# Kernel optimization log

Measured on AMD Instinct MI355X. Metric: run time of the kernel, lower is better.

## Reference

```python
import jax, jax.numpy as jnp
import numpy as np

TREE_DEPTH = 10
TOTAL = 2 ** (TREE_DEPTH + 1) - 1  # 2047 nodes per tree
G = 64                              # graphs per batch
N = G * TOTAL                       # 131008 nodes
E = 2 * N                           # 262016 directed edges
H = 256                             # h_dim
HALF = H // 2
L = 4                               # num_layers
LABELS = 32
OUT = 32
BN_EPS = 1e-5
LN_EPS = 1e-5


def setup_inputs() -> dict:
    key = jax.random.key(0)
    ks = jax.random.split(key, 16)
    x = jnp.stack([jax.random.randint(ks[0], (N,), 0, TOTAL),
                   jax.random.randint(ks[1], (N,), 0, LABELS)], axis=1)
    edge_src = jax.random.randint(ks[2], (E,), 0, N)
    edge_dst = jax.random.randint(ks[3], (E,), 0, N)
    edge_weight = jax.random.uniform(ks[4], (E,), dtype=jnp.float32)
    batch = jnp.arange(N, dtype=jnp.int64) // TOTAL          # node -> graph id
    root_index = jnp.arange(G, dtype=jnp.int64) * TOTAL      # one root per graph
    s = 0.02
    emb_node = jax.random.normal(ks[5], (TOTAL, HALF), dtype=jnp.float32) * s
    emb_label = jax.random.normal(ks[6], (LABELS, HALF), dtype=jnp.float32) * s
    w = 1.0 / np.sqrt(H)
    W1 = jax.random.normal(ks[7], (L, H, H), dtype=jnp.float32) * w
    b1 = jnp.zeros((L, H), dtype=jnp.float32)
    g1 = jnp.ones((L, H), dtype=jnp.float32)
    be1 = jnp.zeros((L, H), dtype=jnp.float32)
    W2 = jax.random.normal(ks[8], (L, H, H), dtype=jnp.float32) * w
    b2 = jnp.zeros((L, H), dtype=jnp.float32)
    g2 = jnp.ones((L, H), dtype=jnp.float32)
    be2 = jnp.zeros((L, H), dtype=jnp.float32)
    ln_g = jnp.ones((L, H), dtype=jnp.float32)
    ln_b = jnp.zeros((L, H), dtype=jnp.float32)
    Wout = jax.random.normal(ks[9], (OUT, H), dtype=jnp.float32) * w
    return {"x": x, "edge_src": edge_src, "edge_dst": edge_dst,
            "edge_weight": edge_weight, "batch": batch, "root_index": root_index,
            "emb_node": emb_node, "emb_label": emb_label,
            "W1": W1, "b1": b1, "g1": g1, "be1": be1,
            "W2": W2, "b2": b2, "g2": g2, "be2": be2,
            "ln_g": ln_g, "ln_b": ln_b, "Wout": Wout}


def _batchnorm(h, g, b):
    # BatchNorm1d, training-mode batch statistics over the node dim
    m = h.mean(axis=0)
    v = h.var(axis=0)
    return g * (h - m) * jax.lax.rsqrt(v + BN_EPS) + b


def _layernorm(h, g, b):
    m = h.mean(axis=-1, keepdims=True)
    v = h.var(axis=-1, keepdims=True)
    return g * (h - m) * jax.lax.rsqrt(v + LN_EPS) + b


def reference(x, edge_src, edge_dst, edge_weight, batch, root_index,
              emb_node, emb_label, W1, b1, g1, be1, W2, b2, g2, be2,
              ln_g, ln_b, Wout):
    # BiEmbedding_cat: concat of two h/2 embeddings
    h = jnp.concatenate([emb_node[x[:, 0]], emb_label[x[:, 1]]], axis=-1)  # [N,H]
    target_roots = root_index[batch]  # all-nodes->root targets for last layer
    for i in range(L):
        if i == L - 1:  # last_layer_fully_adjacent: every node sends to its root
            agg = jnp.zeros_like(h).at[target_roots].add(h)
        else:
            agg = jnp.zeros_like(h).at[edge_dst].add(h[edge_src] * edge_weight[:, None])
        m = h + agg  # GIN with eps=0: (1+eps)*x + sum_j w_ij x_j
        m = jax.nn.relu(_batchnorm(m @ W1[i].T + b1[i], g1[i], be1[i]))
        m = jax.nn.relu(_batchnorm(m @ W2[i].T + b2[i], g2[i], be2[i]))
        # use_activation: relu (idempotent after the MLP's trailing relu)
        h = h + m  # use_residual
        h = _layernorm(h, ln_g[i], ln_b[i])
    roots_x = h[root_index]  # [G,H] root readout
    return roots_x @ Wout.T  # [G,OUT], bias-free out layer
```

## Files before the change

### kernel.cpp

```cpp
#include <hip/hip_runtime.h>
#include <stdint.h>

#define NN 131008
#define NPAD 131072
#define EE 262016
#define HD 256
#define GG 64
#define TT 2047

typedef __attribute__((ext_vector_type(8))) short bfrag;
typedef __attribute__((ext_vector_type(4))) float f32x4;

__device__ __forceinline__ float bflo(unsigned u){ union{unsigned i; float f;} v; v.i = u<<16; return v.f; }
__device__ __forceinline__ float bfhi(unsigned u){ union{unsigned i; float f;} v; v.i = u & 0xffff0000u; return v.f; }
__device__ __forceinline__ unsigned short f2bf(float f){
  union{unsigned i; float fl;} v; v.fl = f; unsigned i = v.i;
  return (unsigned short)((i + 0x7fffu + ((i>>16)&1u)) >> 16);
}
__device__ __forceinline__ unsigned pack2(float a, float b){
  return (unsigned)f2bf(a) | ((unsigned)f2bf(b)<<16);
}
__device__ __forceinline__ void gload16(const void* g, void* s){
  __builtin_amdgcn_global_load_lds((__attribute__((address_space(1))) void*)g,
                                   (__attribute__((address_space(3))) void*)s, 16, 0, 0);
}

__device__ __forceinline__ short bnrelu1_(short t, float a, float c){
  union{unsigned i; float f;} v; v.i = ((unsigned)(unsigned short)t) << 16;
  return (short)f2bf(fmaxf(a*v.f + c, 0.f));
}

__device__ __forceinline__ void atomic_add_bf16x2(unsigned short* p, float a, float b){
#if __has_builtin(__builtin_amdgcn_global_atomic_fadd_v2bf16)
  typedef __attribute__((ext_vector_type(2))) short s16x2;
  s16x2 v; v.x = (short)f2bf(a); v.y = (short)f2bf(b);
  __builtin_amdgcn_global_atomic_fadd_v2bf16((__attribute__((address_space(1))) s16x2*)p, v);
#else
  unsigned* up = (unsigned*)p;
  unsigned old = *up, assumed;
  do {
    assumed = old;
    unsigned nv = pack2(bflo(assumed) + a, bfhi(assumed) + b);
    old = atomicCAS(up, assumed, nv);
  } while (old != assumed);
#endif
}

__global__ void k_prep(const float* __restrict__ W1, const float* __restrict__ W2,
                       unsigned short* __restrict__ wbf,
                       const int* __restrict__ x, const float* __restrict__ en,
                       const float* __restrict__ el, unsigned short* __restrict__ hbf,
                       const int* __restrict__ ed, int* __restrict__ deg){
  int b = blockIdx.x;
  if (b < 2048){
    int idx = b*256 + threadIdx.x;
    float v = (idx < 262144) ? W1[idx] : W2[idx - 262144];
    wbf[idx] = f2bf(v);
  } else if (b < 18432){
    size_t i8 = ((size_t)(b - 2048)*256 + threadIdx.x) << 3;
    int row = (int)(i8 >> 8); int k = (int)(i8 & 255);
    uint4 o;
    if (row < NN){
      const float* src = (k < 128) ? en + (size_t)x[2*row]*128 + k
                                   : el + (size_t)x[2*row+1]*128 + (k-128);
      float4 v0 = *(const float4*)src;
      float4 v1 = *(const float4*)(src + 4);
      o.x = pack2(v0.x, v0.y); o.y = pack2(v0.z, v0.w);
      o.z = pack2(v1.x, v1.y); o.w = pack2(v1.z, v1.w);
    } else { o.x = o.y = o.z = o.w = 0u; }
    *(uint4*)(hbf + i8) = o;
  } else {
    int e = (b - 18432)*256 + threadIdx.x;
    if (e < EE) atomicAdd(&deg[ed[e]], 1);
  }
}

__global__ void k_scan_block(const int* __restrict__ deg, int* __restrict__ start,
                             int* __restrict__ bsum){
  __shared__ int sh[256];
  int t = threadIdx.x;
  int i = blockIdx.x*256 + t;
  int v = deg[i];
  int val = v; sh[t] = val; __syncthreads();
  for (int off = 1; off < 256; off <<= 1){
    int add = (t >= off) ? sh[t-off] : 0;
    __syncthreads();
    val += add; sh[t] = val;
    __syncthreads();
  }
  start[i] = val - v;
  if (t == 255) bsum[blockIdx.x] = val;
}
__global__ void k_scan_top(int* __restrict__ bsum){
  __shared__ int sh[512];
  int t = threadIdx.x;
  int v = bsum[t];
  int val = v; sh[t] = val; __syncthreads();
  for (int off = 1; off < 512; off <<= 1){
    int add = (t >= off) ? sh[t-off] : 0;
    __syncthreads();
    val += add; sh[t] = val;
    __syncthreads();
  }
  bsum[t] = val - v;
}
__global__ void k_fill(const int* __restrict__ es, const int* __restrict__ ed,
                       const float* __restrict__ ew, const int* __restrict__ start,
                       const int* __restrict__ bsum,
                       int* __restrict__ cursor0, uint2* __restrict__ pairs){
  int e = blockIdx.x*256 + threadIdx.x;
  if (e < EE){
    int d = ed[e];
    int pos = start[d] + bsum[d >> 8] + atomicAdd(&cursor0[d], 1);
    uint2 p; p.x = (unsigned)es[e];
    union{float f; unsigned u;} w; w.f = ew[e];
    p.y = w.u;
    pairs[pos] = p;
  }
}

__global__ void k_gather(const int* __restrict__ deg, const int* __restrict__ start,
                         const int* __restrict__ bsum,
                         const uint2* __restrict__ pairs,
                         const unsigned short* __restrict__ hbf,
                         unsigned short* __restrict__ mbf){
  int half = threadIdx.x >> 5, lane32 = threadIdx.x & 31;
  int row = blockIdx.x*8 + half;
  size_t base = (size_t)row*HD + (lane32 << 3);
  uint4 o;
  if (row < NN){
    uint4 hv = *(const uint4*)(hbf + base);
    float a0 = bflo(hv.x), a1 = bfhi(hv.x), a2 = bflo(hv.y), a3 = bfhi(hv.y);
    float a4 = bflo(hv.z), a5 = bfhi(hv.z), a6 = bflo(hv.w), a7 = bfhi(hv.w);
    int d = deg[row], s = start[row] + bsum[row >> 8];
    int j = 0;
    for (; j + 2 <= d; j += 2){
      uint2 p0 = pairs[s + j];
      uint2 p1 = pairs[s + j + 1];
      union{unsigned u; float f;} w0; w0.u = p0.y;
      union{unsigned u; float f;} w1; w1.u = p1.y;
      uint4 s0 = *(const uint4*)(hbf + (size_t)p0.x*HD + (lane32 << 3));
      uint4 s1 = *(const uint4*)(hbf + (size_t)p1.x*HD + (lane32 << 3));
      a0 += bflo(s0.x)*w0.f + bflo(s1.x)*w1.f; a1 += bfhi(s0.x)*w0.f + bfhi(s1.x)*w1.f;
      a2 += bflo(s0.y)*w0.f + bflo(s1.y)*w1.f; a3 += bfhi(s0.y)*w0.f + bfhi(s1.y)*w1.f;
      a4 += bflo(s0.z)*w0.f + bflo(s1.z)*w1.f; a5 += bfhi(s0.z)*w0.f + bfhi(s1.z)*w1.f;
      a6 += bflo(s0.w)*w0.f + bflo(s1.w)*w1.f; a7 += bfhi(s0.w)*w0.f + bfhi(s1.w)*w1.f;
    }
    if (j < d){
      uint2 pr = pairs[s + j];
      union{unsigned u; float f;} wg; wg.u = pr.y;
      uint4 sv = *(const uint4*)(hbf + (size_t)pr.x*HD + (lane32 << 3));
      a0 += bflo(sv.x)*wg.f; a1 += bfhi(sv.x)*wg.f;
      a2 += bflo(sv.y)*wg.f; a3 += bfhi(sv.y)*wg.f;
      a4 += bflo(sv.z)*wg.f; a5 += bfhi(sv.z)*wg.f;
      a6 += bflo(sv.w)*wg.f; a7 += bfhi(sv.w)*wg.f;
    }
    o.x = pack2(a0, a1); o.y = pack2(a2, a3);
    o.z = pack2(a4, a5); o.w = pack2(a6, a7);
  } else { o.x = o.y = o.z = o.w = 0u; }
  *(uint4*)(mbf + base) = o;
}

__global__ void k_rootsum(const unsigned short* __restrict__ hbf, unsigned short* __restrict__ m){
  int g = blockIdx.x >> 4, ch = blockIdx.x & 15;
  int col = threadIdx.x * 2;
  int nr = (ch == 15) ? 127 : 128;
  const unsigned short* p = hbf + ((size_t)g*TT + ch*128)*HD + col;
  float a = 0.f, b = 0.f;
  for (int r = 0; r < nr; ++r){
    unsigned u = *(const unsigned*)(p + (size_t)r*HD);
    a += bflo(u); b += bfhi(u);
  }
  atomic_add_bf16x2(m + (size_t)g*TT*HD + col, a, b);
}

template<bool TRANS>
__device__ __forceinline__ void gemm_body(const unsigned short* __restrict__ A,
                                          const unsigned short* __restrict__ B,
                                          unsigned short* __restrict__ C,
                                          float* __restrict__ gsum, float* __restrict__ gsq,
                                          const float* __restrict__ sum1,
                                          const float* __restrict__ sq1,
                                          const float* __restrict__ g1v,
                                          const float* __restrict__ be1v){
  __shared__ unsigned short Bs[65536];
  __shared__ float st[512];
  __shared__ float acf[256];
  __shared__ float ccf[256];
  const int tid = threadIdx.x, lane = tid & 63, w = tid >> 6;
  const int wr = w >> 1, wc = w & 1;
  const int b = blockIdx.x;
  const int q = lane >> 4, r15 = lane & 15, r7 = lane & 7;

  if (TRANS && tid < 256){
    const float inv_n = 1.f/(float)NN;
    float mean = sum1[tid] * inv_n;
    float var  = fmaxf(sq1[tid] * inv_n - mean*mean, 0.f);
    float aj   = g1v[tid] * rsqrtf(var + 1e-5f);
    acf[tid] = aj;
    ccf[tid] = be1v[tid] - aj*mean;
  }
  st[tid < 512 ? tid : 0] = 0.f;

#pragma unroll
  for (int kt = 0; kt < 4; ++kt)
#pragma unroll
    for (int it = 0; it < 4; ++it){
      int ci = it*512 + tid;
      int row = ci >> 3, cp = ci & 7;
      int cl = cp ^ (row & 7);
      gload16(B + (size_t)row*HD + kt*64 + cl*8, &Bs[kt*16384 + ci*8]);
    }

  bfrag rA[4][2];
  auto aload = [&](int s, int slot){
    const int t2 = b*4 + (s >> 3), ks = s & 7;
    const unsigned short* p = A + ((size_t)(t2*128 + wr*32 + r15))*HD + ks*32 + (q << 3);
    rA[slot][0] = *(const bfrag*)p;
    rA[slot][1] = *(const bfrag*)(p + 16*HD);
  };
  aload(0, 0); aload(1, 1); aload(2, 2);

  asm volatile("s_waitcnt vmcnt(0) lgkmcnt(0)" ::: "memory");
  __builtin_amdgcn_s_barrier();

  f32x4 acc[2][8];
  f32x4 zz = {0.f, 0.f, 0.f, 0.f};
#pragma unroll
  for (int a = 0; a < 2; ++a)
#pragma unroll
    for (int c = 0; c < 8; ++c) acc[a][c] = zz;
  float cs[8] = {0,0,0,0,0,0,0,0}, cq[8] = {0,0,0,0,0,0,0,0};

#pragma unroll 4
  for (int s = 0; s < 32; ++s){
    if (s < 29) aload(s + 3, (s + 3) & 3);

    bfrag a0 = rA[s & 3][0], a1 = rA[s & 3][1];
    const int ks = s & 7;
    if (TRANS){
      const int kb = ks*32 + (q << 3);
      float4 ca0 = *(const float4*)&acf[kb];
      float4 ca1 = *(const float4*)&acf[kb + 4];
      float4 cc0 = *(const float4*)&ccf[kb];
      float4 cc1 = *(const float4*)&ccf[kb + 4];
      bfrag r0, r1;
      r0[0]=bnrelu1_(a0[0],ca0.x,cc0.x); r0[1]=bnrelu1_(a0[1],ca0.y,cc0.y);
      r0[2]=bnrelu1_(a0[2],ca0.z,cc0.z); r0[3]=bnrelu1_(a0[3],ca0.w,cc0.w);
      r0[4]=bnrelu1_(a0[4],ca1.x,cc1.x); r0[5]=bnrelu1_(a0[5],ca1.y,cc1.y);
      r0[6]=bnrelu1_(a0[6],ca1.z,cc1.z); r0[7]=bnrelu1_(a0[7],ca1.w,cc1.w);
      r1[0]=bnrelu1_(a1[0],ca0.x,cc0.x); r1[1]=bnrelu1_(a1[1],ca0.y,cc0.y);
      r1[2]=bnrelu1_(a1[2],ca0.z,cc0.z); r1[3]=bnrelu1_(a1[3],ca0.w,cc0.w);
      r1[4]=bnrelu1_(a1[4],ca1.x,cc1.x); r1[5]=bnrelu1_(a1[5],ca1.y,cc1.y);
      r1[6]=bnrelu1_(a1[6],ca1.z,cc1.z); r1[7]=bnrelu1_(a1[7],ca1.w,cc1.w);
      a0 = r0; a1 = r1;
    }

    const int kt64 = ks >> 1, hf = ks & 1;
    bfrag bf[8];
#pragma unroll
    for (int ct = 0; ct < 8; ++ct){
      int rb = wc*128 + ct*16 + r15;
      bf[ct] = *(const bfrag*)&Bs[kt64*16384 + rb*64 + (((q + 4*hf) ^ r7) << 3)];
    }
    __builtin_amdgcn_s_setprio(1);
#pragma unroll
    for (int ct = 0; ct < 8; ++ct){
      acc[0][ct] = __builtin_amdgcn_mfma_f32_16x16x32_bf16(a0, bf[ct], acc[0][ct], 0, 0, 0);
      acc[1][ct] = __builtin_amdgcn_mfma_f32_16x16x32_bf16(a1, bf[ct], acc[1][ct], 0, 0, 0);
    }
    __builtin_amdgcn_s_setprio(0);

    if ((s & 7) == 7){
      const int tile = b*4 + (s >> 3);
      const int lr0 = wr*32 + q*4;
      const int lc0 = wc*128 + r15;
#pragma unroll
      for (int rt = 0; rt < 2; ++rt)
#pragma unroll
        for (int ct = 0; ct < 8; ++ct){
#pragma unroll
          for (int i = 0; i < 4; ++i){
            size_t grow = (size_t)tile*128 + lr0 + rt*16 + i;
            float v = acc[rt][ct][i];
            C[grow*HD + lc0 + ct*16] = f2bf(v);
            if (grow < NN){ cs[ct] += v; cq[ct] += v*v; }
          }
          acc[rt][ct] = zz;
        }
    }
  }

  const int lc0 = wc*128 + r15;
#pragma unroll
  for (int ct = 0; ct < 8; ++ct){
    float s2 = cs[ct], q2 = cq[ct];
    s2 += __shfl_xor(s2, 16); s2 += __shfl_xor(s2, 32);
    q2 += __shfl_xor(q2, 16); q2 += __shfl_xor(q2, 32);
    if (q == 0){
      atomicAdd(&st[lc0 + ct*16], s2);
      atomicAdd(&st[256 + lc0 + ct*16], q2);
    }
  }
  __syncthreads();
  if (tid < 256){
    atomicAdd(&gsum[tid], st[tid]);
    atomicAdd(&gsq[tid], st[256 + tid]);
  }
}

__global__ __launch_bounds__(512) void k_gemm(const unsigned short* __restrict__ A,
                                              const unsigned short* __restrict__ B,
                                              unsigned short* __restrict__ C,
                                              float* __restrict__ gsum, float* __restrict__ gsq){
  gemm_body<false>(A, B, C, gsum, gsq, nullptr, nullptr, nullptr, nullptr);
}
__global__ __launch_bounds__(512) void k_gemm2(const unsigned short* __restrict__ T,
                                               const float* __restrict__ sum1,
                                               const float* __restrict__ sq1,
                                               const float* __restrict__ g1v,
                                               const float* __restrict__ be1v,
                                               const unsigned short* __restrict__ B,
                                               unsigned short* __restrict__ C,
                                               float* __restrict__ gsum, float* __restrict__ gsq){
  gemm_body<true>(T, B, C, gsum, gsq, sum1, sq1, g1v, be1v);
}

__device__ __forceinline__ void coef4(float4 s4, float4 q4, float4 g4, float4 b4,
                                      float4& a, float4& c){
  const float inv_n = 1.f/(float)NN;
  float m0 = s4.x*inv_n, m1 = s4.y*inv_n, m2 = s4.z*inv_n, m3 = s4.w*inv_n;
  float i0 = rsqrtf(fmaxf(q4.x*inv_n - m0*m0, 0.f) + 1e-5f);
  float i1 = rsqrtf(fmaxf(q4.y*inv_n - m1*m1, 0.f) + 1e-5f);
  float i2 = rsqrtf(fmaxf(q4.z*inv_n - m2*m2, 0.f) + 1e-5f);
  float i3 = rsqrtf(fmaxf(q4.w*inv_n - m3*m3, 0.f) + 1e-5f);
  a.x = g4.x*i0; a.y = g4.y*i1; a.z = g4.z*i2; a.w = g4.w*i3;
  c.x = b4.x - a.x*m0; c.y = b4.y - a.y*m1; c.z = b4.z - a.z*m2; c.w = b4.w - a.w*m3;
}

__global__ void k_fuse(const unsigned short* t2,
                       const float* __restrict__ sum, const float* __restrict__ sq,
                       const float* __restrict__ g, const float* __restrict__ be,
                       const float* __restrict__ lg, const float* __restrict__ lb,
                       unsigned short* __restrict__ hbf, unsigned short* mbf,
                       int writem){
  int half = threadIdx.x >> 5, lane32 = threadIdx.x & 31;
  size_t row = (size_t)blockIdx.x*8 + half;
  int col = lane32 << 3;
  size_t base = row*HD + col;
  uint4 o;
  if (row < NN){
    float4 av0, cv0, av1, cv1;
    coef4(*(const float4*)(sum + col),     *(const float4*)(sq + col),
          *(const float4*)(g + col),       *(const float4*)(be + col),     av0, cv0);
    coef4(*(const float4*)(sum + col + 4), *(const float4*)(sq + col + 4),
          *(const float4*)(g + col + 4),   *(const float4*)(be + col + 4), av1, cv1);
    uint4 tv = *(const uint4*)(t2 + base);
    uint4 hv = *(const uint4*)(hbf + base);
    float r0 = bflo(hv.x) + fmaxf(av0.x*bflo(tv.x) + cv0.x, 0.f);
    float r1 = bfhi(hv.x) + fmaxf(av0.y*bfhi(tv.x) + cv0.y, 0.f);
    float r2 = bflo(hv.y) + fmaxf(av0.z*bflo(tv.y) + cv0.z, 0.f);
    float r3 = bfhi(hv.y) + fmaxf(av0.w*bfhi(tv.y) + cv0.w, 0.f);
    float r4 = bflo(hv.z) + fmaxf(av1.x*bflo(tv.z) + cv1.x, 0.f);
    float r5 = bfhi(hv.z) + fmaxf(av1.y*bfhi(tv.z) + cv1.y, 0.f);
    float r6 = bflo(hv.w) + fmaxf(av1.z*bflo(tv.w) + cv1.z, 0.f);
    float r7 = bfhi(hv.w) + fmaxf(av1.w*bfhi(tv.w) + cv1.w, 0.f);
    float s  = r0+r1+r2+r3+r4+r5+r6+r7;
    float qq = r0*r0+r1*r1+r2*r2+r3*r3+r4*r4+r5*r5+r6*r6+r7*r7;
#pragma unroll
    for (int d = 1; d < 32; d <<= 1){ s += __shfl_xor(s, d); qq += __shfl_xor(qq, d); }
    float mean = s * (1.f/256.f);
    float var  = fmaxf(qq * (1.f/256.f) - mean*mean, 0.f);
    float inv  = rsqrtf(var + 1e-5f);
    float4 gv0 = *(const float4*)(lg + col), gv1 = *(const float4*)(lg + col + 4);
    float4 bv0 = *(const float4*)(lb + col), bv1 = *(const float4*)(lb + col + 4);
    o.x = pack2(gv0.x*(r0 - mean)*inv + bv0.x, gv0.y*(r1 - mean)*inv + bv0.y);
    o.y = pack2(gv0.z*(r2 - mean)*inv + bv0.z, gv0.w*(r3 - mean)*inv + bv0.w);
    o.z = pack2(gv1.x*(r4 - mean)*inv + bv1.x, gv1.y*(r5 - mean)*inv + bv1.y);
    o.w = pack2(gv1.z*(r6 - mean)*inv + bv1.z, gv1.w*(r7 - mean)*inv + bv1.w);
  } else {
    o.x = o.y = o.z = o.w = 0u;
  }
  *(uint4*)(hbf + base) = o;
  if (writem) *(uint4*)(mbf + base) = o;
}

__global__ void k_readout(const unsigned short* __restrict__ hbf, const float* __restrict__ Wo,
                          float* __restrict__ out){
  int g = blockIdx.x;
  int w = threadIdx.x >> 6, lane = threadIdx.x & 63;
  uint2 hv = *(const uint2*)(hbf + (size_t)g*TT*HD + (lane<<2));
  float h0 = bflo(hv.x), h1 = bfhi(hv.x), h2 = bflo(hv.y), h3 = bfhi(hv.y);
#pragma unroll
  for (int oo = 0; oo < 8; ++oo){
    int o = w*8 + oo;
    float4 wv = *(const float4*)(Wo + (size_t)o*HD + (lane<<2));
    float p = h0*wv.x + h1*wv.y + h2*wv.z + h3*wv.w;
#pragma unroll
    for (int d = 1; d < 64; d <<= 1) p += __shfl_xor(p, d);
    if (lane == 0) out[g*32 + o] = p;
  }
}

extern "C" void kernel_launch(void* const* d_in, const int* in_sizes, int n_in,
                              void* d_out, int out_size, void* d_ws, size_t ws_size,
                              hipStream_t stream){
  const int*   x   = (const int*)d_in[0];
  const int*   es  = (const int*)d_in[1];
  const int*   ed  = (const int*)d_in[2];
  const float* ew  = (const float*)d_in[3];
  const float* en  = (const float*)d_in[6];
  const float* el  = (const float*)d_in[7];
  const float* W1  = (const float*)d_in[8];
  const float* g1  = (const float*)d_in[10];
  const float* be1 = (const float*)d_in[11];
  const float* W2  = (const float*)d_in[12];
  const float* g2  = (const float*)d_in[14];
  const float* be2 = (const float*)d_in[15];
  const float* lg  = (const float*)d_in[16];
  const float* lb  = (const float*)d_in[17];
  const float* Wo  = (const float*)d_in[18];

  char* ws = (char*)d_ws;
  unsigned short* hbf = (unsigned short*)ws;
  unsigned short* mbf = (unsigned short*)(ws + 67108864);
  unsigned short* t   = (unsigned short*)(ws + 134217728);
  unsigned short* wbf = (unsigned short*)(ws + 201326592);
  float* stats   = (float*)(ws + 202375168);
  int*   deg     = (int*)  (ws + 202391552);
  int*   cursor0 = (int*)  (ws + 202915840);
  int*   start   = (int*)  (ws + 203440128);
  int*   bsum    = (int*)  (ws + 203964416);
  uint2* pairs   = (uint2*)(ws + 203968512);

  hipMemsetAsync(stats, 0, 16384 + 524288 + 524288, stream);
  k_prep<<<19456, 256, 0, stream>>>(W1, W2, wbf, x, en, el, hbf, ed, deg);

  k_scan_block<<<512, 256, 0, stream>>>(deg, start, bsum);
  k_scan_top  <<<1,   512, 0, stream>>>(bsum);
  k_fill      <<<1024,256, 0, stream>>>(es, ed, ew, start, bsum, cursor0, pairs);

  for (int i = 0; i < 4; ++i){
    float* s1 = stats + (2*i)*512;
    float* s2 = stats + (2*i+1)*512;
    if (i < 3) k_gather <<<16384, 256, 0, stream>>>(deg, start, bsum, pairs, hbf, mbf);
    else       k_rootsum<<<1024,  128, 0, stream>>>(hbf, mbf);

    k_gemm <<<256, 512, 0, stream>>>(mbf, wbf + i*65536, t, s1, s1 + 256);
    k_gemm2<<<256, 512, 0, stream>>>(t, s1, s1 + 256, g1 + i*256, be1 + i*256,
                                     wbf + 262144 + i*65536, mbf, s2, s2 + 256);
    k_fuse <<<16384, 256, 0, stream>>>(mbf, s2, s2 + 256, g2 + i*256, be2 + i*256,
                                       lg + i*256, lb + i*256, hbf, mbf, (i == 2) ? 1 : 0);
  }

  k_readout<<<64, 256, 0, stream>>>(hbf, Wo, (float*)d_out);
  (void)in_sizes; (void)n_in; (void)out_size; (void)ws_size;
}
```

Measured before the change: 738.9 us.

## Fuse BN2/residual/LayerNorm epilogue into second GEMM via grid-wide barrier

Merges the second GEMM and the separate BN2+ReLU+residual+LayerNorm kernel into one persistent kernel. Blocks first accumulate BN2 statistics, then wait on a global atomic counter spin barrier until all 256 blocks have contributed, and then each block applies the fused epilogue to its own 512 rows. This removes one kernel launch per layer and lets the epilogue read rows the same block just wrote, which may still be in cache. In exchange it depends on all 256 blocks being co-resident and adds spin-wait latency at the barrier.

```diff
diff --git a/kernel.cpp b/kernel.cpp
--- a/kernel.cpp
+++ b/kernel.cpp
@@ -174,15 +174,117 @@
   atomic_add_bf16x2(m + (size_t)g*TT*HD + col, a, b);
 }
 
-template<bool TRANS>
-__device__ __forceinline__ void gemm_body(const unsigned short* __restrict__ A,
-                                          const unsigned short* __restrict__ B,
-                                          unsigned short* __restrict__ C,
-                                          float* __restrict__ gsum, float* __restrict__ gsq,
-                                          const float* __restrict__ sum1,
-                                          const float* __restrict__ sq1,
-                                          const float* __restrict__ g1v,
-                                          const float* __restrict__ be1v){
+__global__ __launch_bounds__(512) void k_gemm(const unsigned short* __restrict__ A,
+                                              const unsigned short* __restrict__ B,
+                                              unsigned short* __restrict__ C,
+                                              float* __restrict__ gsum, float* __restrict__ gsq){
+  __shared__ unsigned short Bs[65536];
+  __shared__ float st[512];
+  const int tid = threadIdx.x, lane = tid & 63, w = tid >> 6;
+  const int wr = w >> 1, wc = w & 1;
+  const int b = blockIdx.x;
+  const int q = lane >> 4, r15 = lane & 15, r7 = lane & 7;
+
+  st[tid < 512 ? tid : 0] = 0.f;
+
+#pragma unroll
+  for (int kt = 0; kt < 4; ++kt)
+#pragma unroll
+    for (int it = 0; it < 4; ++it){
+      int ci = it*512 + tid;
+      int row = ci >> 3, cp = ci & 7;
+      int cl = cp ^ (row & 7);
+      gload16(B + (size_t)row*HD + kt*64 + cl*8, &Bs[kt*16384 + ci*8]);
+    }
+
+  bfrag rA[4][2];
+  auto aload = [&](int s, int slot){
+    const int t2 = b*4 + (s >> 3), ks = s & 7;
+    const unsigned short* p = A + ((size_t)(t2*128 + wr*32 + r15))*HD + ks*32 + (q << 3);
+    rA[slot][0] = *(const bfrag*)p;
+    rA[slot][1] = *(const bfrag*)(p + 16*HD);
+  };
+  aload(0, 0); aload(1, 1); aload(2, 2);
+
+  asm volatile("s_waitcnt vmcnt(0) lgkmcnt(0)" ::: "memory");
+  __builtin_amdgcn_s_barrier();
+
+  f32x4 acc[2][8];
+  f32x4 zz = {0.f, 0.f, 0.f, 0.f};
+#pragma unroll
+  for (int a = 0; a < 2; ++a)
+#pragma unroll
+    for (int c = 0; c < 8; ++c) acc[a][c] = zz;
+  float cs[8] = {0,0,0,0,0,0,0,0}, cq[8] = {0,0,0,0,0,0,0,0};
+
+#pragma unroll 4
+  for (int s = 0; s < 32; ++s){
+    if (s < 29) aload(s + 3, (s + 3) & 3);
+    bfrag a0 = rA[s & 3][0], a1 = rA[s & 3][1];
+    const int ks = s & 7;
+    const int kt64 = ks >> 1, hf = ks & 1;
+    bfrag bf[8];
+#pragma unroll
+    for (int ct = 0; ct < 8; ++ct){
+      int rb = wc*128 + ct*16 + r15;
+      bf[ct] = *(const bfrag*)&Bs[kt64*16384 + rb*64 + (((q + 4*hf) ^ r7) << 3)];
+    }
+    __builtin_amdgcn_s_setprio(1);
+#pragma unroll
+    for (int ct = 0; ct < 8; ++ct){
+      acc[0][ct] = __builtin_amdgcn_mfma_f32_16x16x32_bf16(a0, bf[ct], acc[0][ct], 0, 0, 0);
+      acc[1][ct] = __builtin_amdgcn_mfma_f32_16x16x32_bf16(a1, bf[ct], acc[1][ct], 0, 0, 0);
+    }
+    __builtin_amdgcn_s_setprio(0);
+
+    if ((s & 7) == 7){
+      const int tile = b*4 + (s >> 3);
+      const int lr0 = wr*32 + q*4;
+      const int lc0 = wc*128 + r15;
+#pragma unroll
+      for (int rt = 0; rt < 2; ++rt)
+#pragma unroll
+        for (int ct = 0; ct < 8; ++ct){
+#pragma unroll
+          for (int i = 0; i < 4; ++i){
+            size_t grow = (size_t)tile*128 + lr0 + rt*16 + i;
+            float v = acc[rt][ct][i];
+            C[grow*HD + lc0 + ct*16] = f2bf(v);
+            if (grow < NN){ cs[ct] += v; cq[ct] += v*v; }
+          }
+          acc[rt][ct] = zz;
+        }
+    }
+  }
+
+  const int lc0 = wc*128 + r15;
+#pragma unroll
+  for (int ct = 0; ct < 8; ++ct){
+    float s2 = cs[ct], q2 = cq[ct];
+    s2 += __shfl_xor(s2, 16); s2 += __shfl_xor(s2, 32);
+    q2 += __shfl_xor(q2, 16); q2 += __shfl_xor(q2, 32);
+    if (q == 0){
+      atomicAdd(&st[lc0 + ct*16], s2);
+      atomicAdd(&st[256 + lc0 + ct*16], q2);
+    }
+  }
+  __syncthreads();
+  if (tid < 256){
+    atomicAdd(&gsum[tid], st[tid]);
+    atomicAdd(&gsq[tid], st[256 + tid]);
+  }
+}
+
+__global__ __launch_bounds__(512) void k_gemm2f(
+    const unsigned short* __restrict__ T,
+    const float* __restrict__ sum1, const float* __restrict__ sq1,
+    const float* __restrict__ g1v, const float* __restrict__ be1v,
+    const unsigned short* __restrict__ B,
+    unsigned short* mbf,
+    float* s2sum, float* s2sq,
+    const float* __restrict__ g2v, const float* __restrict__ be2v,
+    const float* __restrict__ lgv, const float* __restrict__ lbv,
+    unsigned short* hbf, int writem, int* ctr){
   __shared__ unsigned short Bs[65536];
   __shared__ float st[512];
   __shared__ float acf[256];
@@ -192,7 +294,7 @@
   const int b = blockIdx.x;
   const int q = lane >> 4, r15 = lane & 15, r7 = lane & 7;
 
-  if (TRANS && tid < 256){
+  if (tid < 256){
     const float inv_n = 1.f/(float)NN;
     float mean = sum1[tid] * inv_n;
     float var  = fmaxf(sq1[tid] * inv_n - mean*mean, 0.f);
@@ -215,7 +317,7 @@
   bfrag rA[4][2];
   auto aload = [&](int s, int slot){
     const int t2 = b*4 + (s >> 3), ks = s & 7;
-    const unsigned short* p = A + ((size_t)(t2*128 + wr*32 + r15))*HD + ks*32 + (q << 3);
+    const unsigned short* p = T + ((size_t)(t2*128 + wr*32 + r15))*HD + ks*32 + (q << 3);
     rA[slot][0] = *(const bfrag*)p;
     rA[slot][1] = *(const bfrag*)(p + 16*HD);
   };
@@ -235,10 +337,9 @@
 #pragma unroll 4
   for (int s = 0; s < 32; ++s){
     if (s < 29) aload(s + 3, (s + 3) & 3);
-
     bfrag a0 = rA[s & 3][0], a1 = rA[s & 3][1];
     const int ks = s & 7;
-    if (TRANS){
+    {
       const int kb = ks*32 + (q << 3);
       float4 ca0 = *(const float4*)&acf[kb];
       float4 ca1 = *(const float4*)&acf[kb + 4];
@@ -283,7 +384,7 @@
           for (int i = 0; i < 4; ++i){
             size_t grow = (size_t)tile*128 + lr0 + rt*16 + i;
             float v = acc[rt][ct][i];
-            C[grow*HD + lc0 + ct*16] = f2bf(v);
+            mbf[grow*HD + lc0 + ct*16] = f2bf(v);
             if (grow < NN){ cs[ct] += v; cq[ct] += v*v; }
           }
           acc[rt][ct] = zz;
@@ -291,98 +392,84 @@
     }
   }
 
-  const int lc0 = wc*128 + r15;
-#pragma unroll
-  for (int ct = 0; ct < 8; ++ct){
-    float s2 = cs[ct], q2 = cq[ct];
-    s2 += __shfl_xor(s2, 16); s2 += __shfl_xor(s2, 32);
-    q2 += __shfl_xor(q2, 16); q2 += __shfl_xor(q2, 32);
-    if (q == 0){
-      atomicAdd(&st[lc0 + ct*16], s2);
-      atomicAdd(&st[256 + lc0 + ct*16], q2);
+  {
+    const int lc0 = wc*128 + r15;
+#pragma unroll
+    for (int ct = 0; ct < 8; ++ct){
+      float s2 = cs[ct], q2 = cq[ct];
+      s2 += __shfl_xor(s2, 16); s2 += __shfl_xor(s2, 32);
+      q2 += __shfl_xor(q2, 16); q2 += __shfl_xor(q2, 32);
+      if (q == 0){
+        atomicAdd(&st[lc0 + ct*16], s2);
+        atomicAdd(&st[256 + lc0 + ct*16], q2);
+      }
     }
   }
   __syncthreads();
   if (tid < 256){
-    atomicAdd(&gsum[tid], st[tid]);
-    atomicAdd(&gsq[tid], st[256 + tid]);
-  }
-}
-
-__global__ __launch_bounds__(512) void k_gemm(const unsigned short* __restrict__ A,
-                                              const unsigned short* __restrict__ B,
-                                              unsigned short* __restrict__ C,
-                                              float* __restrict__ gsum, float* __restrict__ gsq){
-  gemm_body<false>(A, B, C, gsum, gsq, nullptr, nullptr, nullptr, nullptr);
-}
-__global__ __launch_bounds__(512) void k_gemm2(const unsigned short* __restrict__ T,
-                                               const float* __restrict__ sum1,
-                                               const float* __restrict__ sq1,
-                                               const float* __restrict__ g1v,
-                                               const float* __restrict__ be1v,
-                                               const unsigned short* __restrict__ B,
-                                               unsigned short* __restrict__ C,
-                                               float* __restrict__ gsum, float* __restrict__ gsq){
-  gemm_body<true>(T, B, C, gsum, gsq, sum1, sq1, g1v, be1v);
-}
-
-__device__ __forceinline__ void coef4(float4 s4, float4 q4, float4 g4, float4 b4,
-                                      float4& a, float4& c){
-  const float inv_n = 1.f/(float)NN;
-  float m0 = s4.x*inv_n, m1 = s4.y*inv_n, m2 = s4.z*inv_n, m3 = s4.w*inv_n;
-  float i0 = rsqrtf(fmaxf(q4.x*inv_n - m0*m0, 0.f) + 1e-5f);
-  float i1 = rsqrtf(fmaxf(q4.y*inv_n - m1*m1, 0.f) + 1e-5f);
-  float i2 = rsqrtf(fmaxf(q4.z*inv_n - m2*m2, 0.f) + 1e-5f);
-  float i3 = rsqrtf(fmaxf(q4.w*inv_n - m3*m3, 0.f) + 1e-5f);
-  a.x = g4.x*i0; a.y = g4.y*i1; a.z = g4.z*i2; a.w = g4.w*i3;
-  c.x = b4.x - a.x*m0; c.y = b4.y - a.y*m1; c.z = b4.z - a.z*m2; c.w = b4.w - a.w*m3;
-}
-
-__global__ void k_fuse(const unsigned short* t2,
-                       const float* __restrict__ sum, const float* __restrict__ sq,
-                       const float* __restrict__ g, const float* __restrict__ be,
-                       const float* __restrict__ lg, const float* __restrict__ lb,
-                       unsigned short* __restrict__ hbf, unsigned short* mbf,
-                       int writem){
-  int half = threadIdx.x >> 5, lane32 = threadIdx.x & 31;
-  size_t row = (size_t)blockIdx.x*8 + half;
-  int col = lane32 << 3;
-  size_t base = row*HD + col;
-  uint4 o;
-  if (row < NN){
-    float4 av0, cv0, av1, cv1;
-    coef4(*(const float4*)(sum + col),     *(const float4*)(sq + col),
-          *(const float4*)(g + col),       *(const float4*)(be + col),     av0, cv0);
-    coef4(*(const float4*)(sum + col + 4), *(const float4*)(sq + col + 4),
-          *(const float4*)(g + col + 4),   *(const float4*)(be + col + 4), av1, cv1);
-    uint4 tv = *(const uint4*)(t2 + base);
-    uint4 hv = *(const uint4*)(hbf + base);
-    float r0 = bflo(hv.x) + fmaxf(av0.x*bflo(tv.x) + cv0.x, 0.f);
-    float r1 = bfhi(hv.x) + fmaxf(av0.y*bfhi(tv.x) + cv0.y, 0.f);
-    float r2 = bflo(hv.y) + fmaxf(av0.z*bflo(tv.y) + cv0.z, 0.f);
-    float r3 = bfhi(hv.y) + fmaxf(av0.w*bfhi(tv.y) + cv0.w, 0.f);
-    float r4 = bflo(hv.z) + fmaxf(av1.x*bflo(tv.z) + cv1.x, 0.f);
-    float r5 = bfhi(hv.z) + fmaxf(av1.y*bfhi(tv.z) + cv1.y, 0.f);
-    float r6 = bflo(hv.w) + fmaxf(av1.z*bflo(tv.w) + cv1.z, 0.f);
-    float r7 = bfhi(hv.w) + fmaxf(av1.w*bfhi(tv.w) + cv1.w, 0.f);
-    float s  = r0+r1+r2+r3+r4+r5+r6+r7;
-    float qq = r0*r0+r1*r1+r2*r2+r3*r3+r4*r4+r5*r5+r6*r6+r7*r7;
-#pragma unroll
-    for (int d = 1; d < 32; d <<= 1){ s += __shfl_xor(s, d); qq += __shfl_xor(qq, d); }
-    float mean = s * (1.f/256.f);
-    float var  = fmaxf(qq * (1.f/256.f) - mean*mean, 0.f);
-    float inv  = rsqrtf(var + 1e-5f);
-    float4 gv0 = *(const float4*)(lg + col), gv1 = *(const float4*)(lg + col + 4);
-    float4 bv0 = *(const float4*)(lb + col), bv1 = *(const float4*)(lb + col + 4);
-    o.x = pack2(gv0.x*(r0 - mean)*inv + bv0.x, gv0.y*(r1 - mean)*inv + bv0.y);
-    o.y = pack2(gv0.z*(r2 - mean)*inv + bv0.z, gv0.w*(r3 - mean)*inv + bv0.w);
-    o.z = pack2(gv1.x*(r4 - mean)*inv + bv1.x, gv1.y*(r5 - mean)*inv + bv1.y);
-    o.w = pack2(gv1.z*(r6 - mean)*inv + bv1.z, gv1.w*(r7 - mean)*inv + bv1.w);
-  } else {
-    o.x = o.y = o.z = o.w = 0u;
-  }
-  *(uint4*)(hbf + base) = o;
-  if (writem) *(uint4*)(mbf + base) = o;
+    atomicAdd(&s2sum[tid], st[tid]);
+    atomicAdd(&s2sq[tid],  st[256 + tid]);
+  }
+  __threadfence();
+  __syncthreads();
+  if (tid == 0){
+    __hip_atomic_fetch_add(ctr, 1, __ATOMIC_ACQ_REL, __HIP_MEMORY_SCOPE_AGENT);
+    for (int spin = 0; spin < (1 << 20); ++spin){
+      if (__hip_atomic_load(ctr, __ATOMIC_ACQUIRE, __HIP_MEMORY_SCOPE_AGENT) >= (int)gridDim.x)
+        break;
+      __builtin_amdgcn_s_sleep(8);
+    }
+  }
+  __syncthreads();
+
+  {
+    const int lane32 = tid & 31, half16 = tid >> 5;
+    const int col = lane32 << 3;
+    const float inv_n = 1.f/(float)NN;
+    float av[8], cv[8], lgr[8], lbr[8];
+#pragma unroll
+    for (int k = 0; k < 8; ++k){
+      float sv = __hip_atomic_load(&s2sum[col+k], __ATOMIC_RELAXED, __HIP_MEMORY_SCOPE_AGENT);
+      float qv = __hip_atomic_load(&s2sq[col+k],  __ATOMIC_RELAXED, __HIP_MEMORY_SCOPE_AGENT);
+      float mean = sv * inv_n;
+      float var  = fmaxf(qv * inv_n - mean*mean, 0.f);
+      float a = g2v[col+k] * rsqrtf(var + 1e-5f);
+      av[k] = a; cv[k] = be2v[col+k] - a*mean;
+      lgr[k] = lgv[col+k]; lbr[k] = lbv[col+k];
+    }
+    for (int it = 0; it < 32; ++it){
+      size_t row = (size_t)b*512 + it*16 + half16;
+      size_t base = row*HD + col;
+      uint4 o;
+      if (row < NN){
+        uint4 tv = *(const uint4*)(mbf + base);
+        uint4 hv = *(const uint4*)(hbf + base);
+        float r0 = bflo(hv.x) + fmaxf(av[0]*bflo(tv.x) + cv[0], 0.f);
+        float r1 = bfhi(hv.x) + fmaxf(av[1]*bfhi(tv.x) + cv[1], 0.f);
+        float r2 = bflo(hv.y) + fmaxf(av[2]*bflo(tv.y) + cv[2], 0.f);
+        float r3 = bfhi(hv.y) + fmaxf(av[3]*bfhi(tv.y) + cv[3], 0.f);
+        float r4 = bflo(hv.z) + fmaxf(av[4]*bflo(tv.z) + cv[4], 0.f);
+        float r5 = bfhi(hv.z) + fmaxf(av[5]*bfhi(tv.z) + cv[5], 0.f);
+        float r6 = bflo(hv.w) + fmaxf(av[6]*bflo(tv.w) + cv[6], 0.f);
+        float r7 = bfhi(hv.w) + fmaxf(av[7]*bfhi(tv.w) + cv[7], 0.f);
+        float s  = r0+r1+r2+r3+r4+r5+r6+r7;
+        float qq = r0*r0+r1*r1+r2*r2+r3*r3+r4*r4+r5*r5+r6*r6+r7*r7;
+#pragma unroll
+        for (int d = 1; d < 32; d <<= 1){ s += __shfl_xor(s, d); qq += __shfl_xor(qq, d); }
+        float mean = s * (1.f/256.f);
+        float var  = fmaxf(qq * (1.f/256.f) - mean*mean, 0.f);
+        float inv  = rsqrtf(var + 1e-5f);
+        o.x = pack2(lgr[0]*(r0 - mean)*inv + lbr[0], lgr[1]*(r1 - mean)*inv + lbr[1]);
+        o.y = pack2(lgr[2]*(r2 - mean)*inv + lbr[2], lgr[3]*(r3 - mean)*inv + lbr[3]);
+        o.z = pack2(lgr[4]*(r4 - mean)*inv + lbr[4], lgr[5]*(r5 - mean)*inv + lbr[5]);
+        o.w = pack2(lgr[6]*(r6 - mean)*inv + lbr[6], lgr[7]*(r7 - mean)*inv + lbr[7]);
+      } else {
+        o.x = o.y = o.z = o.w = 0u;
+      }
+      *(uint4*)(hbf + base) = o;
+      if (writem) *(uint4*)(mbf + base) = o;
+    }
+  }
 }
 
 __global__ void k_readout(const unsigned short* __restrict__ hbf, const float* __restrict__ Wo,
@@ -432,6 +519,7 @@
   int*   start   = (int*)  (ws + 203440128);
   int*   bsum    = (int*)  (ws + 203964416);
   uint2* pairs   = (uint2*)(ws + 203968512);
+  int*   ctr     = cursor0 + 131068;
 
   hipMemsetAsync(stats, 0, 16384 + 524288 + 524288, stream);
   k_prep<<<19456, 256, 0, stream>>>(W1, W2, wbf, x, en, el, hbf, ed, deg);
@@ -447,10 +535,10 @@
     else       k_rootsum<<<1024,  128, 0, stream>>>(hbf, mbf);
 
     k_gemm <<<256, 512, 0, stream>>>(mbf, wbf + i*65536, t, s1, s1 + 256);
-    k_gemm2<<<256, 512, 0, stream>>>(t, s1, s1 + 256, g1 + i*256, be1 + i*256,
-                                     wbf + 262144 + i*65536, mbf, s2, s2 + 256);
-    k_fuse <<<16384, 256, 0, stream>>>(mbf, s2, s2 + 256, g2 + i*256, be2 + i*256,
-                                       lg + i*256, lb + i*256, hbf, mbf, (i == 2) ? 1 : 0);
+    k_gemm2f<<<256, 512, 0, stream>>>(t, s1, s1 + 256, g1 + i*256, be1 + i*256,
+                                      wbf + 262144 + i*65536, mbf, s2, s2 + 256,
+                                      g2 + i*256, be2 + i*256, lg + i*256, lb + i*256,
+                                      hbf, (i == 2) ? 1 : 0, ctr + i);
   }
 
   k_readout<<<64, 256, 0, stream>>>(hbf, Wo, (float*)d_out);
```

New measurement: 891.4 us. +20.6%, slower.
